# Performance work log

Measured on AMD Instinct MI355X. Metric: run time of the kernel, lower is better.

## Reference

```python
import jax, jax.numpy as jnp
import numpy as np

SPATIAL_SHAPES = np.array([[100, 100], [50, 50], [25, 25], [13, 13]], dtype=np.int64)
LEVEL_START = np.concatenate([[0], np.cumsum(SPATIAL_SHAPES[:, 0] * SPATIAL_SHAPES[:, 1])[:-1]])
L_TOK = int((SPATIAL_SHAPES[:, 0] * SPATIAL_SHAPES[:, 1]).sum())  # 13294
B, D_MODEL, N_HEADS, N_LEVELS, N_POINTS, D_FFN = 4, 256, 8, 4, 4, 1024
HEAD_DIM = D_MODEL // N_HEADS


def setup_inputs() -> dict:
    key = jax.random.key(0)
    ks = jax.random.split(key, 16)
    p = lambda k, s: jax.random.normal(k, s, jnp.float32) * 0.02
    return {
        'src': jax.random.normal(ks[0], (B, L_TOK, D_MODEL), jnp.float32),
        'src2': jax.random.normal(ks[1], (B, L_TOK, D_MODEL), jnp.float32),
        'pos': jax.random.normal(ks[2], (B, L_TOK, D_MODEL), jnp.float32),
        'memory_pos': jax.random.normal(ks[3], (B, L_TOK, D_MODEL), jnp.float32),
        'value_w': p(ks[4], (D_MODEL, D_MODEL)), 'value_b': jnp.zeros((D_MODEL,), jnp.float32),
        'off_w': p(ks[5], (D_MODEL, N_HEADS * N_LEVELS * N_POINTS * 2)),
        'off_b': p(ks[6], (N_HEADS * N_LEVELS * N_POINTS * 2,)),
        'aw_w': p(ks[7], (D_MODEL, N_HEADS * N_LEVELS * N_POINTS)),
        'aw_b': jnp.zeros((N_HEADS * N_LEVELS * N_POINTS,), jnp.float32),
        'out_w': p(ks[8], (D_MODEL, D_MODEL)), 'out_b': jnp.zeros((D_MODEL,), jnp.float32),
        'ln_g': jnp.ones((D_MODEL,), jnp.float32), 'ln_b': jnp.zeros((D_MODEL,), jnp.float32),
        'lin1_w': p(ks[9], (D_MODEL, D_FFN)), 'lin1_b': jnp.zeros((D_FFN,), jnp.float32),
        'lin2_w': p(ks[10], (D_FFN, D_MODEL)), 'lin2_b': jnp.zeros((D_MODEL,), jnp.float32),
    }


def _layer_norm(x, g, b, eps=1e-5):
    mu = jnp.mean(x, -1, keepdims=True)
    var = jnp.mean(jnp.square(x - mu), -1, keepdims=True)
    return (x - mu) * jax.lax.rsqrt(var + eps) * g + b


def _reference_points():
    # per get_reference_points: normalized (x, y) centers per src level -> [1, L_TOK, 1, 2]
    pts = []
    for H_, W_ in SPATIAL_SHAPES:
        ry, rx = np.meshgrid(np.linspace(0.5, H_ - 0.5, H_) / H_,
                             np.linspace(0.5, W_ - 0.5, W_) / W_, indexing='ij')
        pts.append(np.stack([rx.reshape(-1), ry.reshape(-1)], -1))
    return jnp.asarray(np.concatenate(pts, 0), jnp.float32)[None, :, None, :]


def _bilinear(value, loc, H_, W_):
    # value: [N, H*W, D]; loc: [N, S, 2] normalized in [0,1]
    # matches F.grid_sample(align_corners=False, padding_mode='zeros') with grid = 2*loc-1
    x = loc[..., 0] * W_ - 0.5
    y = loc[..., 1] * H_ - 0.5
    x0 = jnp.floor(x)
    y0 = jnp.floor(y)
    wx1 = x - x0
    wy1 = y - y0
    out = jnp.zeros(value.shape[:1] + loc.shape[1:2] + value.shape[2:], value.dtype)
    for dy, wy in ((0, 1.0 - wy1), (1, wy1)):
        for dx, wx in ((0, 1.0 - wx1), (1, wx1)):
            xi = x0 + dx
            yi = y0 + dy
            valid = (xi >= 0) & (xi < W_) & (yi >= 0) & (yi < H_)
            idx = (jnp.clip(yi, 0, H_ - 1) * W_ + jnp.clip(xi, 0, W_ - 1)).astype(jnp.int32)
            v = jnp.take_along_axis(value, idx[..., None], axis=1)
            out = out + v * (wx * wy * valid)[..., None]
    return out


def _ms_deform_attn(query, ref, memory, value_w, value_b, off_w, off_b, aw_w, aw_b, out_w, out_b):
    Bq, Lq = query.shape[0], query.shape[1]
    value = (memory @ value_w + value_b).reshape(Bq, -1, N_HEADS, HEAD_DIM)
    offs = (query @ off_w + off_b).reshape(Bq, Lq, N_HEADS, N_LEVELS, N_POINTS, 2)
    norm = jnp.asarray(SPATIAL_SHAPES[:, ::-1].copy(), jnp.float32)  # (W, H) per level
    loc = ref[:, :, None, :, None, :] + offs / norm[None, None, None, :, None, :]
    aw = jax.nn.softmax((query @ aw_w + aw_b).reshape(Bq, Lq, N_HEADS, N_LEVELS * N_POINTS), -1)
    aw = aw.reshape(Bq, Lq, N_HEADS, N_LEVELS, N_POINTS)
    acc = jnp.zeros((Bq, Lq, N_HEADS, HEAD_DIM), query.dtype)
    for l in range(N_LEVELS):
        H_, W_ = int(SPATIAL_SHAPES[l, 0]), int(SPATIAL_SHAPES[l, 1])
        s = int(LEVEL_START[l])
        v = value[:, s:s + H_ * W_].transpose(0, 2, 1, 3).reshape(Bq * N_HEADS, H_ * W_, HEAD_DIM)
        ll = loc[:, :, :, l].transpose(0, 2, 1, 3, 4).reshape(Bq * N_HEADS, Lq * N_POINTS, 2)
        samp = _bilinear(v, ll, H_, W_).reshape(Bq, N_HEADS, Lq, N_POINTS, HEAD_DIM)
        acc = acc + jnp.einsum('bhqpd,bqhp->bqhd', samp, aw[:, :, :, l])
    return acc.reshape(Bq, Lq, D_MODEL) @ out_w + out_b


def reference(src, src2, pos, memory_pos, value_w, value_b, off_w, off_b, aw_w, aw_b,
              out_w, out_b, ln_g, ln_b, lin1_w, lin1_b, lin2_w, lin2_b):
    ref = _reference_points()
    q = src + pos
    mem = src2 + memory_pos
    attn = _ms_deform_attn(q, ref, mem, value_w, value_b, off_w, off_b, aw_w, aw_b, out_w, out_b)
    # residual + norm2 (dropout is identity in eval)
    x = _layer_norm(src + attn, ln_g, ln_b)
    # FFN; note the original re-uses norm2 (it was assigned twice in __init__)
    ffn = jax.nn.relu(x @ lin1_w + lin1_b) @ lin2_w + lin2_b
    return _layer_norm(x + ffn, ln_g, ln_b)
```

## Files before the change

kernel.cpp:

```cpp
#include <hip/hip_runtime.h>
#include <math.h>

#define L_TOKN 13294
#define BATCHN 4
#define NTOK (BATCHN * L_TOKN)
#define NTOKP 53248
#define DMODEL 256
#define DFFN 1024

typedef __attribute__((ext_vector_type(8))) short short8;
typedef __attribute__((ext_vector_type(4))) float f32x4;
typedef __attribute__((ext_vector_type(2))) float f32x2;

__device__ __forceinline__ ushort f2b(float f) {
    uint u = __float_as_uint(f);
    u += 0x7fff + ((u >> 16) & 1);
    return (ushort)(u >> 16);
}
__device__ __forceinline__ float b2f(uint h) {
    return __uint_as_float(h << 16);
}

__global__ __launch_bounds__(256) void prep_k(
    const float* __restrict__ s1, const float* __restrict__ p1,
    const float* __restrict__ s2, const float* __restrict__ p2,
    ushort* __restrict__ o1, ushort* __restrict__ o2,
    const float* __restrict__ w0, const float* __restrict__ w1,
    const float* __restrict__ w2, const float* __restrict__ w3,
    const float* __restrict__ w4, const float* __restrict__ w5,
    ushort* __restrict__ wtb, int n4)
{
    int i = blockIdx.x * 256 + threadIdx.x;
    if (i < 2 * n4) {
        const float* a; const float* b; ushort* o; int j;
        if (i < n4) { a = s1; b = p1; o = o1; j = i; }
        else        { a = s2; b = p2; o = o2; j = i - n4; }
        float4 va = ((const float4*)a)[j];
        float4 vb = ((const float4*)b)[j];
        ushort4 r;
        r.x = f2b(va.x + vb.x); r.y = f2b(va.y + vb.y);
        r.z = f2b(va.z + vb.z); r.w = f2b(va.w + vb.w);
        ((ushort4*)o)[j] = r;
        return;
    }
    int i2 = i - 2 * n4;
    const float* w; int Nd; size_t off; int j;
    if      (i2 < 65536)  { w = w0; Nd = 256;  off = 0;      j = i2; }
    else if (i2 < 131072) { w = w1; Nd = 256;  off = 65536;  j = i2 - 65536; }
    else if (i2 < 163840) { w = w2; Nd = 128;  off = 131072; j = i2 - 131072; }
    else if (i2 < 229376) { w = w3; Nd = 256;  off = 163840; j = i2 - 163840; }
    else if (i2 < 491520) { w = w4; Nd = 1024; off = 229376; j = i2 - 229376; }
    else if (i2 < 753664) { w = w5; Nd = 256;  off = 491520; j = i2 - 491520; }
    else return;
    int Kd = (i2 < 491520) ? 256 : 1024;
    int k = j / Nd, n = j - k * Nd;
    wtb[off + (size_t)n * Kd + k] = f2b(w[j]);
}

__device__ __forceinline__ void gemm_core(
    const ushort* __restrict__ A, const ushort* __restrict__ Wt,
    const float* __restrict__ bias, const float* __restrict__ bias2,
    float* __restrict__ Cf, ushort* __restrict__ Cb,
    int M, int N, int K, int relu, int nsplit, int m0, int n0)
{
    __shared__ ushort lds[12288];

    const int t  = threadIdx.x;
    const int wv = t >> 6, ln_ = t & 63;
    const int fr = ln_ & 15;
    const int kg = ln_ >> 4;

    f32x4 acc[4][2];
    #pragma unroll
    for (int i = 0; i < 4; i++)
        #pragma unroll
        for (int j = 0; j < 2; j++) acc[i][j] = (f32x4)0.0f;

    int aoff[4], boff[2];
    #pragma unroll
    for (int i = 0; i < 4; i++)
        aoff[i] = (i * 16 + fr) * 32 + kg * 8;
    #pragma unroll
    for (int j = 0; j < 2; j++)
        boff[j] = 2048 + (wv * 32 + j * 16 + fr) * 32 + kg * 8;

#define STAGE(pbuf, k0) do {                                                       \
    {                                                   \
        int c = wv * 64 + ln_;                                                     \
        int m = c >> 2, s = c & 3;                                                 \
        const ushort* sa = A + (size_t)(m0 + m) * K + (k0) + s * 8;                \
        __builtin_amdgcn_global_load_lds(                                          \
            (const __attribute__((address_space(1))) unsigned int*)sa,             \
            (__attribute__((address_space(3))) unsigned int*)&lds[(pbuf) * 6144 + wv * 512], \
            16, 0, 0);                                                             \
    }                                                                              \
    _Pragma("unroll")                                                              \
    for (int ii = 0; ii < 2; ii++) {                    \
        int c = wv * 128 + ii * 64 + ln_;                                          \
        int n = c >> 2, s = c & 3;                                                 \
        const ushort* sb = Wt + (size_t)(n0 + n) * K + (k0) + s * 8;               \
        __builtin_amdgcn_global_load_lds(                                          \
            (const __attribute__((address_space(1))) unsigned int*)sb,             \
            (__attribute__((address_space(3))) unsigned int*)&lds[(pbuf) * 6144 + 2048 + wv * 1024 + ii * 512], \
            16, 0, 0);                                                             \
    }                                                                              \
} while (0)

    const int nk = K >> 5;
    STAGE(0, 0);
    if (nk > 1) STAGE(1, 32);

    for (int ks = 0; ks < nk; ks++) {
        const int p = ks & 1;
        if (ks + 1 < nk) {
            asm volatile("s_waitcnt vmcnt(3)" ::: "memory");
        } else {
            asm volatile("s_waitcnt vmcnt(0)" ::: "memory");
        }
        __builtin_amdgcn_s_barrier();
        __builtin_amdgcn_sched_barrier(0);

        short8 af[4], bf[2];
        const int pb = p * 6144;
        #pragma unroll
        for (int i = 0; i < 4; i++)
            af[i] = *(const short8*)&lds[pb + aoff[i]];
        #pragma unroll
        for (int j = 0; j < 2; j++)
            bf[j] = *(const short8*)&lds[pb + boff[j]];

        if (ks + 2 < nk) {
            asm volatile("s_waitcnt lgkmcnt(0)" ::: "memory");
            __builtin_amdgcn_s_barrier();
            __builtin_amdgcn_sched_barrier(0);
            STAGE(p, (ks + 2) << 5);
        }
        #pragma unroll
        for (int i = 0; i < 4; i++)
            #pragma unroll
            for (int j = 0; j < 2; j++)
                acc[i][j] = __builtin_amdgcn_mfma_f32_16x16x32_bf16(af[i], bf[j], acc[i][j], 0, 0, 0);
    }
#undef STAGE

    #pragma unroll
    for (int i = 0; i < 4; i++) {
        #pragma unroll
        for (int j = 0; j < 2; j++) {
            int col = n0 + wv * 32 + j * 16 + fr;
            float bv = (col < nsplit) ? bias[col] : bias2[col - nsplit];
            #pragma unroll
            for (int e = 0; e < 4; e++) {
                int row = m0 + i * 16 + kg * 4 + e;
                if (row >= M) continue;
                float v = acc[i][j][e] + bv;
                if (relu) v = fmaxf(v, 0.f);
                if (Cf) Cf[(size_t)row * N + col] = v;
                if (Cb) Cb[(size_t)row * N + col] = f2b(v);
            }
        }
    }
}

__device__ __forceinline__ int2 xcd_tile(int nx)
{
    int flat  = blockIdx.x + blockIdx.y * gridDim.x;
    int total = gridDim.x * gridDim.y;
    int tile;
    if (total & 7) tile = flat;
    else           tile = (flat & 7) * (total >> 3) + (flat >> 3);
    int2 r; r.x = tile % nx; r.y = tile / nx;
    return r;
}

__global__ __launch_bounds__(256) void mgemm_k(
    const ushort* __restrict__ A, const ushort* __restrict__ Wt,
    const float* __restrict__ bias, const float* __restrict__ bias2,
    float* __restrict__ Cf, ushort* __restrict__ Cb,
    int M, int N, int K, int relu, int nsplit)
{
    int2 xy = xcd_tile(gridDim.x);
    gemm_core(A, Wt, bias, bias2, Cf, Cb, M, N, K, relu, nsplit,
              xy.y * 64, xy.x * 128);
}

__global__ __launch_bounds__(256) void projs_k(
    const ushort* __restrict__ memb, const ushort* __restrict__ qb,
    const ushort* __restrict__ value_wt, const ushort* __restrict__ offaw_wt,
    const float* __restrict__ value_b, const float* __restrict__ off_b,
    const float* __restrict__ aw_b,
    ushort* __restrict__ vb, ushort* __restrict__ offawb)
{
    int2 xy = xcd_tile(5);
    const int x = xy.x;
    const int m0 = xy.y * 64;
    if (x < 2)
        gemm_core(memb, value_wt, value_b, value_b, nullptr, vb,
                  NTOK, 256, 256, 0, 256, m0, x * 128);
    else
        gemm_core(qb, offaw_wt, off_b, aw_b, nullptr, offawb,
                  NTOK, 384, 256, 0, 256, m0, (x - 2) * 128);
}

__global__ __launch_bounds__(256) void deform_k(
    const ushort* __restrict__ Vb,
    const ushort* __restrict__ OFFAW,
    ushort* __restrict__ OUTb)
{
    __shared__ uint4 pw_s[4][2][136];

    const int t = threadIdx.x;
    const int wv = t >> 6, lane = t & 63;
    const int tok0 = blockIdx.x * 8 + wv * 2;

    const int HWc[4] = {100, 50, 25, 13};
    const int STc[4] = {0, 10000, 12500, 13125};

    const int ppb = lane & 15;
    const int lvb = ppb >> 2;
    #pragma unroll
    for (int it = 0; it < 4; it++) {
        int tk = it >> 1;
        int h  = ((it & 1) << 2) + (lane >> 4);
        int row = tok0 + tk;
        int b = row / L_TOKN;
        int l = row - b * L_TOKN;
        int st_q, Wq;
        if      (l < 10000) { st_q = 0;     Wq = 100; }
        else if (l < 12500) { st_q = 10000; Wq = 50;  }
        else if (l < 13125) { st_q = 12500; Wq = 25;  }
        else                { st_q = 13125; Wq = 13;  }
        int li = l - st_q;
        int rowi = li / Wq;
        int coli = li - rowi * Wq;
        float rx = (coli + 0.5f) / (float)Wq;
        float ry = (rowi + 0.5f) / (float)Wq;

        const size_t rbase = (size_t)row * 384;
        uint oxy = *(const uint*)(OFFAW + rbase + h * 32 + ppb * 2);
        float ox = b2f(oxy & 0xffffu);
        float oy = b2f(oxy >> 16);
        float lg = b2f((uint)OFFAW[rbase + 256 + h * 16 + ppb]);
        float mx = lg;
        #pragma unroll
        for (int o = 8; o; o >>= 1) mx = fmaxf(mx, __shfl_xor(mx, o));
        float ex = __expf(lg - mx);
        float sm = ex;
        #pragma unroll
        for (int o = 8; o; o >>= 1) sm += __shfl_xor(sm, o);
        float aw = ex / sm;

        int Wl = HWc[lvb], stl = STc[lvb];
        float Wlf = (float)Wl;
        float x = (rx + ox / Wlf) * Wlf - 0.5f;
        float y = (ry + oy / Wlf) * Wlf - 0.5f;
        float x0f = floorf(x), y0f = floorf(y);
        float wx1 = x - x0f, wy1 = y - y0f;
        float wx0 = 1.f - wx1, wy0 = 1.f - wy1;
        int x0 = (int)x0f, y0 = (int)y0f;
        bool vx0 = (x0 >= 0) & (x0 < Wl);
        bool vx1 = (x0 + 1 >= 0) & (x0 + 1 < Wl);
        bool vy0 = (y0 >= 0) & (y0 < Wl);
        bool vy1 = (y0 + 1 >= 0) & (y0 + 1 < Wl);
        int cx0 = min(max(x0, 0), Wl - 1), cx1 = min(max(x0 + 1, 0), Wl - 1);
        int cy0 = min(max(y0, 0), Wl - 1), cy1 = min(max(y0 + 1, 0), Wl - 1);
        uint gb = (uint)(b * L_TOKN + stl);
        uint i00 = gb + cy0 * Wl + cx0;
        uint i10 = gb + cy0 * Wl + cx1;
        uint i01 = gb + cy1 * Wl + cx0;
        uint i11 = gb + cy1 * Wl + cx1;
        float w00 = wx0 * wy0 * aw * (float)(vx0 & vy0);
        float w10 = wx1 * wy0 * aw * (float)(vx1 & vy0);
        float w01 = wx0 * wy1 * aw * (float)(vx0 & vy1);
        float w11 = wx1 * wy1 * aw * (float)(vx1 & vy1);
        uint4 pk;
        pk.x = (int)(i00 | (i10 << 16));
        pk.y = (int)(i01 | (i11 << 16));
        pk.z = (int)((uint)f2b(w00) | ((uint)f2b(w10) << 16));
        pk.w = (int)((uint)f2b(w01) | ((uint)f2b(w11) << 16));
        pw_s[wv][tk][h * 17 + ppb] = pk;
    }

    asm volatile("s_waitcnt lgkmcnt(0)" ::: "memory");
    __builtin_amdgcn_sched_barrier(0);

    const int tk = lane >> 5;
    const int h  = (lane >> 2) & 7;
    const int dq = lane & 3;
    const int row = tok0 + tk;
    const uint choff = (uint)(h * 64 + dq * 16);
    const char* __restrict__ vbase = (const char*)Vb;

    f32x2 acc2[4];
    #pragma unroll
    for (int k = 0; k < 4; k++) acc2[k] = (f32x2)0.0f;

    #pragma unroll 8
    for (int pq = 0; pq < 16; pq++) {
        uint4 pk = pw_s[wv][tk][h * 17 + pq];
        float w00 = b2f((uint)pk.z & 0xffffu);
        float w10 = __uint_as_float((uint)pk.z & 0xffff0000u);
        float w01 = b2f((uint)pk.w & 0xffffu);
        float w11 = __uint_as_float((uint)pk.w & 0xffff0000u);
        uint a00 = (((uint)pk.x & 0xffffu) << 9) + choff;
        uint a10 = (((uint)pk.x >> 16) << 9) + choff;
        uint a01 = (((uint)pk.y & 0xffffu) << 9) + choff;
        uint a11 = (((uint)pk.y >> 16) << 9) + choff;
        uint4 v00 = *(const uint4*)(vbase + a00);
        uint4 v10 = *(const uint4*)(vbase + a10);
        uint4 v01 = *(const uint4*)(vbase + a01);
        uint4 v11 = *(const uint4*)(vbase + a11);
        const uint* p00 = (const uint*)&v00;
        const uint* p10 = (const uint*)&v10;
        const uint* p01 = (const uint*)&v01;
        const uint* p11 = (const uint*)&v11;
        #pragma unroll
        for (int k = 0; k < 4; k++) {
            f32x2 a0, a1, a2, a3;
            a0.x = __uint_as_float(p00[k] << 16); a0.y = __uint_as_float(p00[k] & 0xffff0000u);
            a1.x = __uint_as_float(p10[k] << 16); a1.y = __uint_as_float(p10[k] & 0xffff0000u);
            a2.x = __uint_as_float(p01[k] << 16); a2.y = __uint_as_float(p01[k] & 0xffff0000u);
            a3.x = __uint_as_float(p11[k] << 16); a3.y = __uint_as_float(p11[k] & 0xffff0000u);
            acc2[k] += a0 * w00 + a1 * w10 + a2 * w01 + a3 * w11;
        }
    }
    ushort4 olo, ohi;
    olo.x = f2b(acc2[0].x); olo.y = f2b(acc2[0].y);
    olo.z = f2b(acc2[1].x); olo.w = f2b(acc2[1].y);
    ohi.x = f2b(acc2[2].x); ohi.y = f2b(acc2[2].y);
    ohi.z = f2b(acc2[3].x); ohi.w = f2b(acc2[3].y);
    ushort* op = OUTb + (size_t)row * 256 + h * 32 + dq * 8;
    *(ushort4*)op = olo;
    *(ushort4*)(op + 4) = ohi;
}

__global__ __launch_bounds__(256) void ln_k(
    const float* __restrict__ af, const ushort* __restrict__ ab,
    const float* __restrict__ bf2, const ushort* __restrict__ bb2,
    const float* __restrict__ g, const float* __restrict__ bta,
    float* __restrict__ of, ushort* __restrict__ ob)
{
    const int r = blockIdx.x * 4 + (threadIdx.x >> 6);
    const int lane = threadIdx.x & 63;
    float4 v;
    if (af) {
        v = *((const float4*)(af + (size_t)r * 256) + lane);
    } else {
        ushort4 u = *((const ushort4*)(ab + (size_t)r * 256) + lane);
        v.x = b2f(u.x); v.y = b2f(u.y); v.z = b2f(u.z); v.w = b2f(u.w);
    }
    if (bf2) {
        float4 v2 = *((const float4*)(bf2 + (size_t)r * 256) + lane);
        v.x += v2.x; v.y += v2.y; v.z += v2.z; v.w += v2.w;
    } else if (bb2) {
        ushort4 u = *((const ushort4*)(bb2 + (size_t)r * 256) + lane);
        v.x += b2f(u.x); v.y += b2f(u.y); v.z += b2f(u.z); v.w += b2f(u.w);
    }
    float s = v.x + v.y + v.z + v.w;
    #pragma unroll
    for (int o = 32; o; o >>= 1) s += __shfl_xor(s, o);
    float mu = s * (1.f / 256.f);
    float4 d; d.x = v.x - mu; d.y = v.y - mu; d.z = v.z - mu; d.w = v.w - mu;
    float s2 = d.x * d.x + d.y * d.y + d.z * d.z + d.w * d.w;
    #pragma unroll
    for (int o = 32; o; o >>= 1) s2 += __shfl_xor(s2, o);
    float rstd = rsqrtf(s2 * (1.f / 256.f) + 1e-5f);
    float4 gg = ((const float4*)g)[lane];
    float4 bb = ((const float4*)bta)[lane];
    float4 out;
    out.x = d.x * rstd * gg.x + bb.x;
    out.y = d.y * rstd * gg.y + bb.y;
    out.z = d.z * rstd * gg.z + bb.z;
    out.w = d.w * rstd * gg.w + bb.w;
    if (of) *((float4*)(of + (size_t)r * 256) + lane) = out;
    if (ob) {
        ushort4 o4;
        o4.x = f2b(out.x); o4.y = f2b(out.y); o4.z = f2b(out.z); o4.w = f2b(out.w);
        *((ushort4*)(ob + (size_t)r * 256) + lane) = o4;
    }
}

extern "C" void kernel_launch(void* const* d_in, const int* in_sizes, int n_in,
                              void* d_out, int out_size, void* d_ws, size_t ws_size,
                              hipStream_t stream)
{
    const float* src     = (const float*)d_in[0];
    const float* src2    = (const float*)d_in[1];
    const float* pos     = (const float*)d_in[2];
    const float* mpos    = (const float*)d_in[3];
    const float* value_w = (const float*)d_in[4];
    const float* value_b = (const float*)d_in[5];
    const float* off_w   = (const float*)d_in[6];
    const float* off_b   = (const float*)d_in[7];
    const float* aw_w    = (const float*)d_in[8];
    const float* aw_b    = (const float*)d_in[9];
    const float* out_w   = (const float*)d_in[10];
    const float* out_b   = (const float*)d_in[11];
    const float* ln_g    = (const float*)d_in[12];
    const float* ln_b    = (const float*)d_in[13];
    const float* lin1_w  = (const float*)d_in[14];
    const float* lin1_b  = (const float*)d_in[15];
    const float* lin2_w  = (const float*)d_in[16];
    const float* lin2_b  = (const float*)d_in[17];

    float* outp = (float*)d_out;
    char*  w8   = (char*)d_ws;

    const size_t SLAB = (size_t)NTOKP * 256 * 2;
    const size_t OASZ = (size_t)NTOKP * 384 * 2;
    const size_t HSZ  = (size_t)NTOKP * 1024 * 2;
    ushort* wtb    = (ushort*)(w8);
    ushort* offawb = (ushort*)(w8 + 1572864);
    ushort* qb     = (ushort*)(w8 + 1572864 + OASZ);
    ushort* vb     = (ushort*)(w8 + 1572864 + OASZ + SLAB);
    ushort* memb   = (ushort*)(w8 + 1572864 + HSZ);
    ushort* attb   = (ushort*)(w8 + 1572864 + HSZ + SLAB);

    ushort* hidb   = offawb;
    ushort* bufXb  = memb;
    ushort* projb  = vb;
    ushort* ffn2b  = attb;

    ushort* value_wt = wtb;
    ushort* offaw_wt = wtb + 65536;
    ushort* out_wt   = wtb + 163840;
    ushort* lin1_wt  = wtb + 229376;
    ushort* lin2_wt  = wtb + 491520;

    const dim3 blk(256);
    const int n4 = NTOK * DMODEL / 4;
    const int prep_total = 2 * n4 + 753664;
    prep_k<<<(prep_total + 255) / 256, blk, 0, stream>>>(
        src, pos, src2, mpos, qb, memb,
        value_w, off_w, aw_w, out_w, lin1_w, lin2_w, wtb, n4);

    const int mt = NTOKP / 64;
    projs_k<<<dim3(5, mt), blk, 0, stream>>>(memb, qb, value_wt, offaw_wt,
                                             value_b, off_b, aw_b, vb, offawb);

    deform_k<<<dim3(NTOK / 8), blk, 0, stream>>>(vb, offawb, attb);

    mgemm_k<<<dim3(2, mt), blk, 0, stream>>>(attb, out_wt, out_b, nullptr,
                                             nullptr, projb, NTOK, 256, 256, 0, 256);
    ln_k<<<dim3(NTOK / 4), blk, 0, stream>>>(nullptr, projb, src, nullptr,
                                             ln_g, ln_b, nullptr, bufXb);

    mgemm_k<<<dim3(8, mt), blk, 0, stream>>>(bufXb, lin1_wt, lin1_b, nullptr,
                                             nullptr, hidb, NTOK, DFFN, DMODEL, 1, DFFN);
    mgemm_k<<<dim3(2, mt), blk, 0, stream>>>(hidb, lin2_wt, lin2_b, nullptr,
                                             nullptr, ffn2b, NTOK, DMODEL, DFFN, 0, DMODEL);

    ln_k<<<dim3(NTOK / 4), blk, 0, stream>>>(nullptr, ffn2b, nullptr, bufXb,
                                             ln_g, ln_b, outp, nullptr);
}
```

Measured before the change: 364.2 us.

## Fuse output-projection and FFN2 GEMMs with residual add and LayerNorm

After: 383.0 us. 1.05x slower.

```diff
diff --git a/kernel.cpp b/kernel.cpp
--- a/kernel.cpp
+++ b/kernel.cpp
@@ -200,6 +200,169 @@
     else
         gemm_core(qb, offaw_wt, off_b, aw_b, nullptr, offawb,
                   NTOK, 384, 256, 0, 256, m0, (x - 2) * 128);
+}
+
+__global__ __launch_bounds__(256) void gemm_ln_k(
+    const ushort* __restrict__ A, const ushort* __restrict__ Wt,
+    const float* __restrict__ bias,
+    const float* __restrict__ resf, const ushort* __restrict__ resb,
+    const float* __restrict__ lng, const float* __restrict__ lnbta,
+    float* __restrict__ outf, ushort* __restrict__ outb, int K)
+{
+    __shared__ ushort lds[20480];
+
+    const int t  = threadIdx.x;
+    const int wv = t >> 6, ln_ = t & 63;
+    const int fr = ln_ & 15;
+    const int kg = ln_ >> 4;
+
+    const int flat = blockIdx.x, total = gridDim.x;
+    const int m0 = ((total & 7) ? flat
+                                : ((flat & 7) * (total >> 3) + (flat >> 3))) * 64;
+
+    f32x4 acc[4][4];
+    #pragma unroll
+    for (int i = 0; i < 4; i++)
+        #pragma unroll
+        for (int j = 0; j < 4; j++) acc[i][j] = (f32x4)0.0f;
+
+    int aoff[4], boff[4];
+    #pragma unroll
+    for (int i = 0; i < 4; i++)
+        aoff[i] = (i * 16 + fr) * 32 + kg * 8;
+    #pragma unroll
+    for (int j = 0; j < 4; j++)
+        boff[j] = 2048 + (wv * 64 + j * 16 + fr) * 32 + kg * 8;
+
+#define STAGE2(pbuf, k0) do {                                                      \
+    {                                                   \
+        int c = wv * 64 + ln_;                                                     \
+        int m = c >> 2, s = c & 3;                                                 \
+        const ushort* sa = A + (size_t)(m0 + m) * K + (k0) + s * 8;                \
+        __builtin_amdgcn_global_load_lds(                                          \
+            (const __attribute__((address_space(1))) unsigned int*)sa,             \
+            (__attribute__((address_space(3))) unsigned int*)&lds[(pbuf) * 10240 + wv * 512], \
+            16, 0, 0);                                                             \
+    }                                                                              \
+    _Pragma("unroll")                                                              \
+    for (int ii = 0; ii < 4; ii++) {                   \
+        int c = wv * 256 + ii * 64 + ln_;                                          \
+        int n = c >> 2, s = c & 3;                                                 \
+        const ushort* sb = Wt + (size_t)n * K + (k0) + s * 8;                      \
+        __builtin_amdgcn_global_load_lds(                                          \
+            (const __attribute__((address_space(1))) unsigned int*)sb,             \
+            (__attribute__((address_space(3))) unsigned int*)&lds[(pbuf) * 10240 + 2048 + wv * 2048 + ii * 512], \
+            16, 0, 0);                                                             \
+    }                                                                              \
+} while (0)
+
+    const int nk = K >> 5;
+    STAGE2(0, 0);
+    STAGE2(1, 32);
+
+    for (int ks = 0; ks < nk; ks++) {
+        const int p = ks & 1;
+        if (ks + 1 < nk) {
+            asm volatile("s_waitcnt vmcnt(5)" ::: "memory");
+        } else {
+            asm volatile("s_waitcnt vmcnt(0)" ::: "memory");
+        }
+        __builtin_amdgcn_s_barrier();
+        __builtin_amdgcn_sched_barrier(0);
+
+        short8 af[4], bf[4];
+        const int pb = p * 10240;
+        #pragma unroll
+        for (int i = 0; i < 4; i++)
+            af[i] = *(const short8*)&lds[pb + aoff[i]];
+        #pragma unroll
+        for (int j = 0; j < 4; j++)
+            bf[j] = *(const short8*)&lds[pb + boff[j]];
+
+        if (ks + 2 < nk) {
+            asm volatile("s_waitcnt lgkmcnt(0)" ::: "memory");
+            __builtin_amdgcn_s_barrier();
+            __builtin_amdgcn_sched_barrier(0);
+            STAGE2(p, (ks + 2) << 5);
+        }
+        #pragma unroll
+        for (int i = 0; i < 4; i++)
+            #pragma unroll
+            for (int j = 0; j < 4; j++)
+                acc[i][j] = __builtin_amdgcn_mfma_f32_16x16x32_bf16(af[i], bf[j], acc[i][j], 0, 0, 0);
+    }
+#undef STAGE2
+
+    #pragma unroll
+    for (int i = 0; i < 4; i++) {
+        #pragma unroll
+        for (int j = 0; j < 4; j++) {
+            int col = wv * 64 + j * 16 + fr;
+            float bv = bias[col];
+            #pragma unroll
+            for (int e = 0; e < 4; e++) {
+                size_t idx = (size_t)(m0 + i * 16 + kg * 4 + e) * 256 + col;
+                float r = resf ? resf[idx] : b2f((uint)resb[idx]);
+                acc[i][j][e] += bv + r;
+            }
+        }
+    }
+
+    float s1[16], s2[16];
+    #pragma unroll
+    for (int i = 0; i < 4; i++)
+        #pragma unroll
+        for (int e = 0; e < 4; e++) {
+            float a = acc[i][0][e], b = acc[i][1][e];
+            float c = acc[i][2][e], d = acc[i][3][e];
+            s1[i * 4 + e] = a + b + c + d;
+            s2[i * 4 + e] = a * a + b * b + c * c + d * d;
+        }
+    #pragma unroll
+    for (int o = 8; o; o >>= 1) {
+        #pragma unroll
+        for (int r = 0; r < 16; r++) {
+            s1[r] += __shfl_xor(s1[r], o);
+            s2[r] += __shfl_xor(s2[r], o);
+        }
+    }
+
+    float* sumS = (float*)lds;
+    float* sqS  = (float*)lds + 256;
+    __syncthreads();
+    if (fr == 0) {
+        #pragma unroll
+        for (int i = 0; i < 4; i++)
+            #pragma unroll
+            for (int e = 0; e < 4; e++) {
+                int r = i * 16 + kg * 4 + e;
+                sumS[wv * 64 + r] = s1[i * 4 + e];
+                sqS[wv * 64 + r]  = s2[i * 4 + e];
+            }
+    }
+    __syncthreads();
+
+    #pragma unroll
+    for (int i = 0; i < 4; i++) {
+        #pragma unroll
+        for (int e = 0; e < 4; e++) {
+            int r = i * 16 + kg * 4 + e;
+            float tS = sumS[r] + sumS[64 + r] + sumS[128 + r] + sumS[192 + r];
+            float tQ = sqS[r]  + sqS[64 + r]  + sqS[128 + r]  + sqS[192 + r];
+            float mu = tS * (1.f / 256.f);
+            float var = tQ * (1.f / 256.f) - mu * mu;
+            float rstd = rsqrtf(var + 1e-5f);
+            int row = m0 + i * 16 + kg * 4 + e;
+            if (row >= NTOK) continue;
+            #pragma unroll
+            for (int j = 0; j < 4; j++) {
+                int col = wv * 64 + j * 16 + fr;
+                float o = (acc[i][j][e] - mu) * rstd * lng[col] + lnbta[col];
+                if (outf) outf[(size_t)row * 256 + col] = o;
+                if (outb) outb[(size_t)row * 256 + col] = f2b(o);
+            }
+        }
+    }
 }
 
 __global__ __launch_bounds__(256) void deform_k(
@@ -334,52 +497,6 @@
     *(ushort4*)(op + 4) = ohi;
 }
 
-__global__ __launch_bounds__(256) void ln_k(
-    const float* __restrict__ af, const ushort* __restrict__ ab,
-    const float* __restrict__ bf2, const ushort* __restrict__ bb2,
-    const float* __restrict__ g, const float* __restrict__ bta,
-    float* __restrict__ of, ushort* __restrict__ ob)
-{
-    const int r = blockIdx.x * 4 + (threadIdx.x >> 6);
-    const int lane = threadIdx.x & 63;
-    float4 v;
-    if (af) {
-        v = *((const float4*)(af + (size_t)r * 256) + lane);
-    } else {
-        ushort4 u = *((const ushort4*)(ab + (size_t)r * 256) + lane);
-        v.x = b2f(u.x); v.y = b2f(u.y); v.z = b2f(u.z); v.w = b2f(u.w);
-    }
-    if (bf2) {
-        float4 v2 = *((const float4*)(bf2 + (size_t)r * 256) + lane);
-        v.x += v2.x; v.y += v2.y; v.z += v2.z; v.w += v2.w;
-    } else if (bb2) {
-        ushort4 u = *((const ushort4*)(bb2 + (size_t)r * 256) + lane);
-        v.x += b2f(u.x); v.y += b2f(u.y); v.z += b2f(u.z); v.w += b2f(u.w);
-    }
-    float s = v.x + v.y + v.z + v.w;
-    #pragma unroll
-    for (int o = 32; o; o >>= 1) s += __shfl_xor(s, o);
-    float mu = s * (1.f / 256.f);
-    float4 d; d.x = v.x - mu; d.y = v.y - mu; d.z = v.z - mu; d.w = v.w - mu;
-    float s2 = d.x * d.x + d.y * d.y + d.z * d.z + d.w * d.w;
-    #pragma unroll
-    for (int o = 32; o; o >>= 1) s2 += __shfl_xor(s2, o);
-    float rstd = rsqrtf(s2 * (1.f / 256.f) + 1e-5f);
-    float4 gg = ((const float4*)g)[lane];
-    float4 bb = ((const float4*)bta)[lane];
-    float4 out;
-    out.x = d.x * rstd * gg.x + bb.x;
-    out.y = d.y * rstd * gg.y + bb.y;
-    out.z = d.z * rstd * gg.z + bb.z;
-    out.w = d.w * rstd * gg.w + bb.w;
-    if (of) *((float4*)(of + (size_t)r * 256) + lane) = out;
-    if (ob) {
-        ushort4 o4;
-        o4.x = f2b(out.x); o4.y = f2b(out.y); o4.z = f2b(out.z); o4.w = f2b(out.w);
-        *((ushort4*)(ob + (size_t)r * 256) + lane) = o4;
-    }
-}
-
 extern "C" void kernel_launch(void* const* d_in, const int* in_sizes, int n_in,
                               void* d_out, int out_size, void* d_ws, size_t ws_size,
                               hipStream_t stream)
@@ -418,8 +535,6 @@
 
     ushort* hidb   = offawb;
     ushort* bufXb  = memb;
-    ushort* projb  = vb;
-    ushort* ffn2b  = attb;
 
     ushort* value_wt = wtb;
     ushort* offaw_wt = wtb + 65536;
@@ -440,16 +555,14 @@
 
     deform_k<<<dim3(NTOK / 8), blk, 0, stream>>>(vb, offawb, attb);
 
-    mgemm_k<<<dim3(2, mt), blk, 0, stream>>>(attb, out_wt, out_b, nullptr,
-                                             nullptr, projb, NTOK, 256, 256, 0, 256);
-    ln_k<<<dim3(NTOK / 4), blk, 0, stream>>>(nullptr, projb, src, nullptr,
-                                             ln_g, ln_b, nullptr, bufXb);
+    gemm_ln_k<<<dim3(mt), blk, 0, stream>>>(attb, out_wt, out_b,
+                                            src, nullptr, ln_g, ln_b,
+                                            nullptr, bufXb, 256);
 
     mgemm_k<<<dim3(8, mt), blk, 0, stream>>>(bufXb, lin1_wt, lin1_b, nullptr,
                                              nullptr, hidb, NTOK, DFFN, DMODEL, 1, DFFN);
-    mgemm_k<<<dim3(2, mt), blk, 0, stream>>>(hidb, lin2_wt, lin2_b, nullptr,
-                                             nullptr, ffn2b, NTOK, DMODEL, DFFN, 0, DMODEL);
-
-    ln_k<<<dim3(NTOK / 4), blk, 0, stream>>>(nullptr, ffn2b, nullptr, bufXb,
-                                             ln_g, ln_b, outp, nullptr);
-}
+
+    gemm_ln_k<<<dim3(mt), blk, 0, stream>>>(hidb, lin2_wt, lin2_b,
+                                            nullptr, bufXb, ln_g, ln_b,
+                                            outp, nullptr, 1024);
+}
```
